# Optimization experiments

Measured on AMD Instinct MI355X. Metric: run time of the kernel, lower is better.

Reference implementation:

```python
import jax, jax.numpy as jnp
import numpy as np

IRE = 1.0 / 400.0

def _stencil(f):
    # f: [B, C, X, Y]; returns (u,v) 5-point stencil fields, each [B, X-2, Y-2]
    m = f[:, :, 1:-1, 1:-1]
    l = f[:, :, :-2, 1:-1]
    r = f[:, :, 2:, 1:-1]
    b = f[:, :, 1:-1, :-2]
    t = f[:, :, 1:-1, 2:]
    return (m[:, 0], m[:, 1], l[:, 0], l[:, 1], r[:, 0], r[:, 1],
            b[:, 0], b[:, 1], t[:, 0], t[:, 1])

def _residuals(um, vm, ul, vl, ur, vr, ub, vb, ut, vt):
    dudx = (ur - ul) * 0.5
    dvdy = (vt - vb) * 0.5
    dudy = (ut - ub) * 0.5
    dvdx = (vr - vl) * 0.5
    du2dx = 0.25 * ((ur + um) ** 2 - (ul + um) ** 2)
    duvdy = 0.25 * ((ut + um) * (vt + vm) - (ub + um) * (vb + vm))
    dv2dy = 0.25 * ((vt + vm) ** 2 - (vb + vm) ** 2)
    dvudx = 0.25 * ((vr + vm) * (ur + um) - (vl + vm) * (ul + um))
    dudx2 = ur - um * 2 + ul
    dudy2 = ut - um * 2 + ub
    dvdx2 = vr - vm * 2 + vl
    dvdy2 = vt - vm * 2 + vb
    mass = dudx + dvdy
    mom_u = du2dx + duvdy - (dudx2 + dudy2) * IRE
    mom_v = dvudx + dv2dy - (dvdx2 + dvdy2) * IRE
    return mass, mom_u, mom_v, dudx, dudy, dvdx, dvdy

def setup_inputs() -> dict:
    key = jax.random.key(0)
    k1, k2 = jax.random.split(key)
    pred = jax.random.normal(k1, (64, 2, 512, 512), dtype=jnp.float32)
    trut = jax.random.normal(k2, (64, 2, 512, 512), dtype=jnp.float32)
    return {"pred": pred, "trut": trut}

def reference(pred, trut):
    mass_t, momu_t, momv_t, dudx_t, dudy_t, dvdx_t, dvdy_t = _residuals(*_stencil(trut))
    mass_p, momu_p, momv_p, dudx_p, dudy_p, dvdx_p, dvdy_p = _residuals(*_stencil(pred))
    lossMass = jnp.mean(jnp.abs(mass_t - mass_p))
    lossMom = jnp.mean(jnp.abs(momu_t - momu_p) + jnp.abs(momv_t - momv_p))
    lossGdl = jnp.mean(jnp.abs(dudx_t - dudx_p) + jnp.abs(dudy_t - dudy_p)
                       + jnp.abs(dvdx_t - dvdx_p) + jnp.abs(dvdy_t - dvdy_p)) / 4.0
    lossL1 = jnp.mean(jnp.abs(pred - trut))
    # lossGdl computed (as in original) but unused in the final combination
    del lossGdl
    return (lossMass * 5 + lossMom * 25 + lossL1) / 3
```

## Files before the change

kernel.cpp:

```cpp
#include <hip/hip_runtime.h>

#define IRE (1.0f / 400.0f)

constexpr int W  = 512;
constexpr int H  = 512;
constexpr int NB = 64;
constexpr int TR = 32;
constexpr int TILES = H / TR;
constexpr int NBLK  = NB * TILES;
constexpr int NSLOT = 5;


__device__ __forceinline__ void residuals3(
    float um, float vm, float ul, float vl, float ur, float vr,
    float ub, float vb, float ut, float vt,
    float& mass, float& momu, float& momv)
{
    float dudx = (ur - ul) * 0.5f;
    float dvdy = (vt - vb) * 0.5f;
    float ru = ur + um, lu = ul + um, tu_ = ut + um, bu = ub + um;
    float rv = vr + vm, lv = vl + vm, tv_ = vt + vm, bv = vb + vm;
    float du2dx = 0.25f * (ru * ru - lu * lu);
    float duvdy = 0.25f * (tu_ * tv_ - bu * bv);
    float dv2dy = 0.25f * (tv_ * tv_ - bv * bv);
    float dvudx = 0.25f * (rv * ru - lv * lu);
    float dudx2 = ur - 2.0f * um + ul;
    float dudy2 = ut - 2.0f * um + ub;
    float dvdx2 = vr - 2.0f * vm + vl;
    float dvdy2 = vt - 2.0f * vm + vb;
    mass = dudx + dvdy;
    momu = du2dx + duvdy - (dudx2 + dudy2) * IRE;
    momv = dvudx + dv2dy - (dvdx2 + dvdy2) * IRE;
}

__global__ __launch_bounds__(256, 4) void loss_main(
    const float* __restrict__ pred, const float* __restrict__ trut,
    double* __restrict__ partial)
{
    __shared__ __align__(16) float ring[NSLOT * 4 * W];

    const int tid  = (int)threadIdx.x;
    const int lane = tid & 63;
    const int wv   = tid >> 6;
    const int blk  = (int)blockIdx.x;
    const int tile = blk % TILES;
    const int b    = blk / TILES;
    const int r0   = tile * TR;

    const size_t CH = (size_t)H * W;
    const float* gbase = (wv < 2 ? trut : pred) + (size_t)b * 2 * CH + (size_t)(wv & 1) * CH;

    auto stage_row = [&](int row, int slot) {
        row = row < 0 ? 0 : (row > H - 1 ? H - 1 : row);
        const float* src = gbase + (size_t)row * W + lane * 4;
        float* dst = &ring[slot * (4 * W) + wv * W];
        __builtin_amdgcn_global_load_lds(
            (const __attribute__((address_space(1))) void*)src,
            (__attribute__((address_space(3))) void*)dst, 16, 0, 0);
        __builtin_amdgcn_global_load_lds(
            (const __attribute__((address_space(1))) void*)(src + 256),
            (__attribute__((address_space(3))) void*)(dst + 256), 16, 0, 0);
    };

    stage_row(r0 - 1, 0);
    stage_row(r0,     1);
    stage_row(r0 + 1, 2);
    stage_row(r0 + 2, 3);

    const int j0  = tid * 2;
    const int jm1 = (j0 == 0) ? 0 : j0 - 1;
    const int jp2 = (j0 + 2 > W - 1) ? W - 1 : j0 + 2;

    float accMass = 0.0f, accMom = 0.0f, accL1 = 0.0f;

    float2 topc[4], midc[4], botc[4];
    float  midl[4], midr[4], botl[4], botr[4];

    asm volatile("s_waitcnt vmcnt(4)\n\ts_barrier" ::: "memory");
    #pragma unroll
    for (int a = 0; a < 4; ++a) {
        const float* p0 = &ring[0 * (4 * W) + a * W];
        const float* p1 = &ring[1 * (4 * W) + a * W];
        topc[a] = *(const float2*)(p0 + j0);
        midc[a] = *(const float2*)(p1 + j0);
        midl[a] = p1[jm1];
        midr[a] = p1[jp2];
    }

    int sBot = 2, sStage = 4;
    #pragma unroll 4
    for (int s = 0; s < TR; ++s) {
        const int r = r0 + s;
        if (s < TR - 2) {
            stage_row(r + 3, sStage);
            asm volatile("s_waitcnt vmcnt(4) lgkmcnt(0)\n\ts_barrier" ::: "memory");
        } else if (s == TR - 2) {
            asm volatile("s_waitcnt vmcnt(2) lgkmcnt(0)\n\ts_barrier" ::: "memory");
        } else {
            asm volatile("s_waitcnt vmcnt(0) lgkmcnt(0)\n\ts_barrier" ::: "memory");
        }

        const float* bp = &ring[sBot * (4 * W)];
        #pragma unroll
        for (int a = 0; a < 4; ++a) {
            botc[a] = *(const float2*)(bp + a * W + j0);
            botl[a] = bp[a * W + jm1];
            botr[a] = bp[a * W + jp2];
        }

        accL1 += fabsf(midc[2].x - midc[0].x) + fabsf(midc[2].y - midc[0].y)
               + fabsf(midc[3].x - midc[1].x) + fabsf(midc[3].y - midc[1].y);

        if (r >= 1 && r <= H - 2) {
            float mT, uT, vT, mP, uP, vP;
            residuals3(midc[0].x, midc[1].x, topc[0].x, topc[1].x, botc[0].x, botc[1].x,
                       midl[0],   midl[1],   midc[0].y, midc[1].y, mT, uT, vT);
            residuals3(midc[2].x, midc[3].x, topc[2].x, topc[3].x, botc[2].x, botc[3].x,
                       midl[2],   midl[3],   midc[2].y, midc[3].y, mP, uP, vP);
            if (j0 >= 1) {
                accMass += fabsf(mT - mP);
                accMom  += fabsf(uT - uP) + fabsf(vT - vP);
            }
            residuals3(midc[0].y, midc[1].y, topc[0].y, topc[1].y, botc[0].y, botc[1].y,
                       midc[0].x, midc[1].x, midr[0],   midr[1],   mT, uT, vT);
            residuals3(midc[2].y, midc[3].y, topc[2].y, topc[3].y, botc[2].y, botc[3].y,
                       midc[2].x, midc[3].x, midr[2],   midr[3],   mP, uP, vP);
            if (j0 + 1 <= W - 2) {
                accMass += fabsf(mT - mP);
                accMom  += fabsf(uT - uP) + fabsf(vT - vP);
            }
        }

        #pragma unroll
        for (int a = 0; a < 4; ++a) {
            topc[a] = midc[a];
            midc[a] = botc[a];
            midl[a] = botl[a];
            midr[a] = botr[a];
        }
        sBot   = (sBot   == NSLOT - 1) ? 0 : sBot + 1;
        sStage = (sStage == NSLOT - 1) ? 0 : sStage + 1;
    }

    float res = 5.0f * accMass + 25.0f * accMom;
    float l1  = accL1;
    #pragma unroll
    for (int off = 32; off > 0; off >>= 1) {
        res += __shfl_down(res, off);
        l1  += __shfl_down(l1, off);
    }
    __syncthreads();
    double* sred = (double*)ring;
    if (lane == 0) { sred[wv] = (double)res; sred[4 + wv] = (double)l1; }
    __syncthreads();
    if (tid == 0) {
        partial[(size_t)blk * 2 + 0] = sred[0] + sred[1] + sred[2] + sred[3];
        partial[(size_t)blk * 2 + 1] = sred[4] + sred[5] + sred[6] + sred[7];
    }
}

__global__ __launch_bounds__(256) void loss_final(
    const double* __restrict__ partial, float* __restrict__ out)
{
    __shared__ double sres[4], sl1[4];
    const int t = (int)threadIdx.x;
    double res = 0.0, l1 = 0.0;
    for (int i = t; i < NBLK; i += 256) {
        res += partial[(size_t)i * 2 + 0];
        l1  += partial[(size_t)i * 2 + 1];
    }
    #pragma unroll
    for (int off = 32; off > 0; off >>= 1) {
        res += __shfl_down(res, off);
        l1  += __shfl_down(l1, off);
    }
    const int wave = t >> 6;
    if ((t & 63) == 0) { sres[wave] = res; sl1[wave] = l1; }
    __syncthreads();
    if (t == 0) {
        res = sres[0] + sres[1] + sres[2] + sres[3];
        l1  = sl1[0] + sl1[1] + sl1[2] + sl1[3];
        const double nRes = 64.0 * 510.0 * 510.0;
        const double nL1  = 64.0 * 2.0 * 512.0 * 512.0;
        out[0] = (float)((res / nRes + l1 / nL1) / 3.0);
    }
}

extern "C" void kernel_launch(void* const* d_in, const int* in_sizes, int n_in,
                              void* d_out, int out_size, void* d_ws, size_t ws_size,
                              hipStream_t stream)
{
    const float* pred = (const float*)d_in[0];
    const float* trut = (const float*)d_in[1];
    double* partial = (double*)d_ws;
    loss_main<<<NBLK, 256, 0, stream>>>(pred, trut, partial);
    loss_final<<<1, 256, 0, stream>>>(partial, (float*)d_out);
}
```

Measured before the change: 284.8 us.

## Use 512 threads per block with one column per thread and four-slot ring

```diff
diff --git a/kernel.cpp b/kernel.cpp
--- a/kernel.cpp
+++ b/kernel.cpp
@@ -8,7 +8,8 @@
 constexpr int TR = 32;
 constexpr int TILES = H / TR;
 constexpr int NBLK  = NB * TILES;
-constexpr int NSLOT = 5;
+constexpr int TPB   = 512;
+constexpr int NSLOT = 4;
 
 
 __device__ __forceinline__ void residuals3(
@@ -33,7 +34,7 @@
     momv = dvudx + dv2dy - (dvdx2 + dvdy2) * IRE;
 }
 
-__global__ __launch_bounds__(256, 4) void loss_main(
+__global__ __launch_bounds__(TPB, 8) void loss_main(
     const float* __restrict__ pred, const float* __restrict__ trut,
     double* __restrict__ partial)
 {
@@ -42,24 +43,23 @@
     const int tid  = (int)threadIdx.x;
     const int lane = tid & 63;
     const int wv   = tid >> 6;
+    const int arr  = wv >> 1;
+    const int half = wv & 1;
     const int blk  = (int)blockIdx.x;
     const int tile = blk % TILES;
     const int b    = blk / TILES;
     const int r0   = tile * TR;
 
     const size_t CH = (size_t)H * W;
-    const float* gbase = (wv < 2 ? trut : pred) + (size_t)b * 2 * CH + (size_t)(wv & 1) * CH;
+    const float* gbase = (arr < 2 ? trut : pred) + (size_t)b * 2 * CH + (size_t)(arr & 1) * CH;
 
     auto stage_row = [&](int row, int slot) {
         row = row < 0 ? 0 : (row > H - 1 ? H - 1 : row);
-        const float* src = gbase + (size_t)row * W + lane * 4;
-        float* dst = &ring[slot * (4 * W) + wv * W];
+        const float* src = gbase + (size_t)row * W + half * 256 + lane * 4;
+        float* dst = &ring[slot * (4 * W) + arr * W + half * 256];
         __builtin_amdgcn_global_load_lds(
             (const __attribute__((address_space(1))) void*)src,
             (__attribute__((address_space(3))) void*)dst, 16, 0, 0);
-        __builtin_amdgcn_global_load_lds(
-            (const __attribute__((address_space(1))) void*)(src + 256),
-            (__attribute__((address_space(3))) void*)(dst + 256), 16, 0, 0);
     };
 
     stage_row(r0 - 1, 0);
@@ -67,35 +67,35 @@
     stage_row(r0 + 1, 2);
     stage_row(r0 + 2, 3);
 
-    const int j0  = tid * 2;
+    const int j0  = tid;
     const int jm1 = (j0 == 0) ? 0 : j0 - 1;
-    const int jp2 = (j0 + 2 > W - 1) ? W - 1 : j0 + 2;
+    const int jp1 = (j0 == W - 1) ? W - 1 : j0 + 1;
 
     float accMass = 0.0f, accMom = 0.0f, accL1 = 0.0f;
 
-    float2 topc[4], midc[4], botc[4];
-    float  midl[4], midr[4], botl[4], botr[4];
+    float tc[4], ml[4], mc[4], mr[4], bl[4], bc[4], br[4];
 
-    asm volatile("s_waitcnt vmcnt(4)\n\ts_barrier" ::: "memory");
+    asm volatile("s_waitcnt vmcnt(2)\n\ts_barrier" ::: "memory");
     #pragma unroll
     for (int a = 0; a < 4; ++a) {
         const float* p0 = &ring[0 * (4 * W) + a * W];
         const float* p1 = &ring[1 * (4 * W) + a * W];
-        topc[a] = *(const float2*)(p0 + j0);
-        midc[a] = *(const float2*)(p1 + j0);
-        midl[a] = p1[jm1];
-        midr[a] = p1[jp2];
+        tc[a] = p0[j0];
+        ml[a] = p1[jm1];
+        mc[a] = p1[j0];
+        mr[a] = p1[jp1];
     }
+    asm volatile("s_waitcnt lgkmcnt(0)\n\ts_barrier" ::: "memory");
 
-    int sBot = 2, sStage = 4;
+    int sBot = 2, sStage = 0;
     #pragma unroll 4
     for (int s = 0; s < TR; ++s) {
         const int r = r0 + s;
         if (s < TR - 2) {
             stage_row(r + 3, sStage);
-            asm volatile("s_waitcnt vmcnt(4) lgkmcnt(0)\n\ts_barrier" ::: "memory");
+            asm volatile("s_waitcnt vmcnt(2) lgkmcnt(0)\n\ts_barrier" ::: "memory");
         } else if (s == TR - 2) {
-            asm volatile("s_waitcnt vmcnt(2) lgkmcnt(0)\n\ts_barrier" ::: "memory");
+            asm volatile("s_waitcnt vmcnt(1) lgkmcnt(0)\n\ts_barrier" ::: "memory");
         } else {
             asm volatile("s_waitcnt vmcnt(0) lgkmcnt(0)\n\ts_barrier" ::: "memory");
         }
@@ -103,29 +103,20 @@
         const float* bp = &ring[sBot * (4 * W)];
         #pragma unroll
         for (int a = 0; a < 4; ++a) {
-            botc[a] = *(const float2*)(bp + a * W + j0);
-            botl[a] = bp[a * W + jm1];
-            botr[a] = bp[a * W + jp2];
+            bl[a] = bp[a * W + jm1];
+            bc[a] = bp[a * W + j0];
+            br[a] = bp[a * W + jp1];
         }
 
-        accL1 += fabsf(midc[2].x - midc[0].x) + fabsf(midc[2].y - midc[0].y)
-               + fabsf(midc[3].x - midc[1].x) + fabsf(midc[3].y - midc[1].y);
+        accL1 += fabsf(mc[2] - mc[0]) + fabsf(mc[3] - mc[1]);
 
         if (r >= 1 && r <= H - 2) {
             float mT, uT, vT, mP, uP, vP;
-            residuals3(midc[0].x, midc[1].x, topc[0].x, topc[1].x, botc[0].x, botc[1].x,
-                       midl[0],   midl[1],   midc[0].y, midc[1].y, mT, uT, vT);
-            residuals3(midc[2].x, midc[3].x, topc[2].x, topc[3].x, botc[2].x, botc[3].x,
-                       midl[2],   midl[3],   midc[2].y, midc[3].y, mP, uP, vP);
-            if (j0 >= 1) {
-                accMass += fabsf(mT - mP);
-                accMom  += fabsf(uT - uP) + fabsf(vT - vP);
-            }
-            residuals3(midc[0].y, midc[1].y, topc[0].y, topc[1].y, botc[0].y, botc[1].y,
-                       midc[0].x, midc[1].x, midr[0],   midr[1],   mT, uT, vT);
-            residuals3(midc[2].y, midc[3].y, topc[2].y, topc[3].y, botc[2].y, botc[3].y,
-                       midc[2].x, midc[3].x, midr[2],   midr[3],   mP, uP, vP);
-            if (j0 + 1 <= W - 2) {
+            residuals3(mc[0], mc[1], tc[0], tc[1], bc[0], bc[1],
+                       ml[0], ml[1], mr[0], mr[1], mT, uT, vT);
+            residuals3(mc[2], mc[3], tc[2], tc[3], bc[2], bc[3],
+                       ml[2], ml[3], mr[2], mr[3], mP, uP, vP);
+            if (j0 >= 1 && j0 <= W - 2) {
                 accMass += fabsf(mT - mP);
                 accMom  += fabsf(uT - uP) + fabsf(vT - vP);
             }
@@ -133,13 +124,13 @@
 
         #pragma unroll
         for (int a = 0; a < 4; ++a) {
-            topc[a] = midc[a];
-            midc[a] = botc[a];
-            midl[a] = botl[a];
-            midr[a] = botr[a];
+            tc[a] = mc[a];
+            ml[a] = bl[a];
+            mc[a] = bc[a];
+            mr[a] = br[a];
         }
-        sBot   = (sBot   == NSLOT - 1) ? 0 : sBot + 1;
-        sStage = (sStage == NSLOT - 1) ? 0 : sStage + 1;
+        sBot   = (sBot   + 1) & 3;
+        sStage = (sStage + 1) & 3;
     }
 
     float res = 5.0f * accMass + 25.0f * accMom;
@@ -151,11 +142,14 @@
     }
     __syncthreads();
     double* sred = (double*)ring;
-    if (lane == 0) { sred[wv] = (double)res; sred[4 + wv] = (double)l1; }
+    if (lane == 0) { sred[wv] = (double)res; sred[8 + wv] = (double)l1; }
     __syncthreads();
     if (tid == 0) {
-        partial[(size_t)blk * 2 + 0] = sred[0] + sred[1] + sred[2] + sred[3];
-        partial[(size_t)blk * 2 + 1] = sred[4] + sred[5] + sred[6] + sred[7];
+        double resS = 0.0, l1S = 0.0;
+        #pragma unroll
+        for (int i = 0; i < 8; ++i) { resS += sred[i]; l1S += sred[8 + i]; }
+        partial[(size_t)blk * 2 + 0] = resS;
+        partial[(size_t)blk * 2 + 1] = l1S;
     }
 }
 
@@ -193,6 +187,6 @@
     const float* pred = (const float*)d_in[0];
     const float* trut = (const float*)d_in[1];
     double* partial = (double*)d_ws;
-    loss_main<<<NBLK, 256, 0, stream>>>(pred, trut, partial);
+    loss_main<<<NBLK, TPB, 0, stream>>>(pred, trut, partial);
     loss_final<<<1, 256, 0, stream>>>(partial, (float*)d_out);
 }
```

After: 283.0 us. About the same (-0.6%).
